# Optimization experiments

Hardware: AMD Instinct MI355X
Metric: run time of the kernel (lower is better)

## Reference

```python
import jax, jax.numpy as jnp
import numpy as np

ALPHA = 0.1
K = 10
N_NODES = 100000
N_EDGES = 3200000


def setup_inputs() -> dict:
    key = jax.random.key(0)
    ks = jax.random.split(key, 8)
    feat = jax.random.normal(ks[0], (N_NODES, 512), dtype=jnp.float32)
    W1 = jax.random.normal(ks[1], (512, 256), dtype=jnp.float32) * (1.0 / np.sqrt(512))
    b1 = jnp.zeros((256,), dtype=jnp.float32)
    W2 = jax.random.normal(ks[2], (256, 64), dtype=jnp.float32) * (1.0 / np.sqrt(256))
    b2 = jnp.zeros((64,), dtype=jnp.float32)
    edge_vals = jax.random.uniform(ks[3], (N_EDGES,), dtype=jnp.float32) / 32.0  # ~row-normalized
    edge_row = jax.random.randint(ks[4], (N_EDGES,), 0, N_NODES, dtype=jnp.int32)
    edge_col = jax.random.randint(ks[5], (N_EDGES,), 0, N_NODES, dtype=jnp.int32)
    return {"features": feat, "W1": W1, "b1": b1, "W2": W2, "b2": b2,
            "edge_vals": edge_vals, "edge_row": edge_row, "edge_col": edge_col}


def _spmm(edge_vals, edge_row, edge_col, x):
    # out[r] = sum_e vals[e] * x[col[e]]  for edges with row[e]==r
    msgs = edge_vals[:, None] * x[edge_col]  # [E, C]
    return jax.ops.segment_sum(msgs, edge_row, num_segments=N_NODES)


def reference(features, W1, b1, W2, b2, edge_vals, edge_row, edge_col):
    # MLP (dropout is identity in eval mode)
    x = jax.nn.relu(features @ W1 + b1)        # [N, nhid]
    x = x @ W2 + b2                             # [N, num_classes]
    h = x
    for _ in range(K):
        x = (1.0 - ALPHA) * _spmm(edge_vals, edge_row, edge_col, x) + ALPHA * h
    return jax.nn.log_softmax(x, axis=1)
```

## Files before the change

kernel.cpp:

```cpp
#include <hip/hip_runtime.h>
#include <hip/hip_bf16.h>
#include <math.h>

#define NNODES 100000
#define NFEAT 512
#define NHID 256
#define NCLS 64
#define ALPHA_C 0.1f
#define NBUCKET 512
#define NPB 512
#define RB2 196

typedef short s16x8 __attribute__((ext_vector_type(8)));
typedef float f32x4 __attribute__((ext_vector_type(4)));

__device__ inline unsigned short f2b(float f) {
    union { float f; unsigned u; } v; v.f = f;
    unsigned r = v.u + 0x7fff + ((v.u >> 16) & 1);
    return (unsigned short)(r >> 16);
}
__device__ inline float b2f(unsigned short b) {
    return __uint_as_float((unsigned)b << 16);
}
__device__ inline float blo(unsigned u) { return __uint_as_float(u << 16); }
__device__ inline float bhi(unsigned u) { return __uint_as_float(u & 0xffff0000u); }

__global__ __launch_bounds__(256) void cvtT_kernel(
    const float* __restrict__ src, unsigned short* __restrict__ dst, int R, int Clog2)
{
    int idx = blockIdx.x * 256 + threadIdx.x;
    int C = 1 << Clog2;
    if (idx < R * C) {
        int r = idx >> Clog2, c = idx & (C - 1);
        dst[(size_t)c * R + r] = f2b(src[idx]);
    }
}

#define HID_STRIDE 264

__global__ __launch_bounds__(256) void mlp_mfma_kernel(
    const float* __restrict__ feat, const unsigned short* __restrict__ W1T,
    const float* __restrict__ b1, const unsigned short* __restrict__ W2T,
    const float* __restrict__ b2, unsigned short* __restrict__ h, int N)
{
    __shared__ unsigned short hid_s[64 * HID_STRIDE];
    const int tid  = threadIdx.x;
    const int w    = tid >> 6;
    const int lane = tid & 63;
    const int lr   = lane & 15;
    const int lh   = lane >> 4;
    const int m0   = blockIdx.x * 64;

    f32x4 acc[4][4];
#pragma unroll
    for (int i = 0; i < 4; ++i)
#pragma unroll
        for (int j = 0; j < 4; ++j) acc[i][j] = (f32x4)0.f;

    const float* arow[4];
#pragma unroll
    for (int mi = 0; mi < 4; ++mi) {
        int r = m0 + mi * 16 + lr;
        if (r > N - 1) r = N - 1;
        arow[mi] = feat + (size_t)r * NFEAT;
    }
    const unsigned short* brow[4];
#pragma unroll
    for (int nj = 0; nj < 4; ++nj)
        brow[nj] = W1T + (size_t)(w * 64 + nj * 16 + lr) * NFEAT;

    for (int kb = 0; kb < NFEAT; kb += 32) {
        const int k0 = kb + lh * 8;
        s16x8 afr[4], bfr[4];
#pragma unroll
        for (int mi = 0; mi < 4; ++mi) {
            float4 f0 = *reinterpret_cast<const float4*>(arow[mi] + k0);
            float4 f1 = *reinterpret_cast<const float4*>(arow[mi] + k0 + 4);
            s16x8 a;
            a[0] = f2b(f0.x); a[1] = f2b(f0.y); a[2] = f2b(f0.z); a[3] = f2b(f0.w);
            a[4] = f2b(f1.x); a[5] = f2b(f1.y); a[6] = f2b(f1.z); a[7] = f2b(f1.w);
            afr[mi] = a;
        }
#pragma unroll
        for (int nj = 0; nj < 4; ++nj)
            bfr[nj] = *reinterpret_cast<const s16x8*>(brow[nj] + k0);
#pragma unroll
        for (int mi = 0; mi < 4; ++mi)
#pragma unroll
            for (int nj = 0; nj < 4; ++nj)
                acc[mi][nj] = __builtin_amdgcn_mfma_f32_16x16x32_bf16(
                    afr[mi], bfr[nj], acc[mi][nj], 0, 0, 0);
    }

#pragma unroll
    for (int nj = 0; nj < 4; ++nj) {
        int col = w * 64 + nj * 16 + lr;
        float bias = b1[col];
#pragma unroll
        for (int mi = 0; mi < 4; ++mi)
#pragma unroll
            for (int q = 0; q < 4; ++q) {
                int row = mi * 16 + lh * 4 + q;
                hid_s[row * HID_STRIDE + col] = f2b(fmaxf(acc[mi][nj][q] + bias, 0.f));
            }
    }
    __syncthreads();

    f32x4 acc2[4];
#pragma unroll
    for (int i = 0; i < 4; ++i) acc2[i] = (f32x4)0.f;
    const int cw = w * 16;
    const unsigned short* b2row = W2T + (size_t)(cw + lr) * NHID;
    for (int ks = 0; ks < NHID; ks += 32) {
        int k0 = ks + lh * 8;
        s16x8 bfr = *reinterpret_cast<const s16x8*>(b2row + k0);
#pragma unroll
        for (int mi = 0; mi < 4; ++mi) {
            s16x8 afr = *reinterpret_cast<const s16x8*>(
                &hid_s[(mi * 16 + lr) * HID_STRIDE + k0]);
            acc2[mi] = __builtin_amdgcn_mfma_f32_16x16x32_bf16(afr, bfr, acc2[mi], 0, 0, 0);
        }
    }
    int col = cw + lr;
    float bias2 = b2[col];
#pragma unroll
    for (int mi = 0; mi < 4; ++mi)
#pragma unroll
        for (int q = 0; q < 4; ++q) {
            int row = m0 + mi * 16 + lh * 4 + q;
            if (row < N) h[(size_t)row * NCLS + col] = f2b(acc2[mi][q] + bias2);
        }
}

__global__ __launch_bounds__(1024) void scanA_kernel(
    const int* __restrict__ cnt, int* __restrict__ excl, int* __restrict__ partials, int n)
{
    __shared__ int wsum[16];
    const int t = threadIdx.x, wid = t >> 6, lane = t & 63;
    const int i = blockIdx.x * 1024 + t;
    int c = (i < n) ? cnt[i] : 0;
    int x = c;
#pragma unroll
    for (int off = 1; off < 64; off <<= 1) {
        int y = __shfl_up(x, off);
        if (lane >= off) x += y;
    }
    if (lane == 63) wsum[wid] = x;
    __syncthreads();
    if (wid == 0 && lane < 16) {
        int wv = wsum[lane];
#pragma unroll
        for (int off = 1; off < 16; off <<= 1) {
            int y = __shfl_up(wv, off);
            if (lane >= off) wv += y;
        }
        wsum[lane] = wv;
    }
    __syncthreads();
    int woff = wid ? wsum[wid - 1] : 0;
    int incl = x + woff;
    if (i < n) excl[i] = incl - c;
    if (t == 1023) partials[blockIdx.x] = incl;
}

__global__ __launch_bounds__(256) void scanB_kernel(
    int* __restrict__ partials, int* __restrict__ total_out, int nb, int n)
{
    __shared__ int s[256];
    const int t = threadIdx.x;
    int v = (t < nb) ? partials[t] : 0;
    s[t] = v;
    __syncthreads();
    for (int off = 1; off < 256; off <<= 1) {
        int y = (t >= off) ? s[t - off] : 0;
        __syncthreads();
        s[t] += y;
        __syncthreads();
    }
    partials[t] = s[t] - v;
    if (t == 255) total_out[n] = s[255];
}

__global__ __launch_bounds__(1024) void scanC_kernel(
    int* __restrict__ arr, const int* __restrict__ partials, int n)
{
    const int i = blockIdx.x * 1024 + threadIdx.x;
    if (i < n) arr[i] += partials[blockIdx.x];
}

__global__ __launch_bounds__(256) void countP1_kernel(
    const int* __restrict__ erow, int* __restrict__ cnts, int E, int CE)
{
    __shared__ int c[NBUCKET];
    const int blk = blockIdx.x, t = threadIdx.x;
    for (int i = t; i < NBUCKET; i += 256) c[i] = 0;
    __syncthreads();
    const int e0 = blk * CE, e1 = min(e0 + CE, E);
    for (int e = e0 + t; e < e1; e += 256)
        atomicAdd(&c[erow[e] / RB2], 1);
    __syncthreads();
    for (int b = t; b < NBUCKET; b += 256)
        cnts[(size_t)b * NPB + blk] = c[b];
}

__global__ __launch_bounds__(256) void scatterA_kernel(
    const float* __restrict__ vals, const int* __restrict__ erow,
    const int* __restrict__ ecol, const int* __restrict__ S,
    unsigned long long* __restrict__ stage, int E, int CE)
{
    __shared__ int lcur[NBUCKET];
    const int blk = blockIdx.x, t = threadIdx.x;
    for (int b = t; b < NBUCKET; b += 256) lcur[b] = S[(size_t)b * NPB + blk];
    __syncthreads();
    const int e0 = blk * CE, e1 = min(e0 + CE, E);
    for (int e = e0 + t; e < e1; e += 256) {
        int r = erow[e];
        unsigned q = (unsigned)__float2int_rn(vals[e] * 1048576.f);
        if (q > 32767u) q = 32767u;
        unsigned lo = ((unsigned)ecol[e] << 15) | q;
        int pos = atomicAdd(&lcur[r / RB2], 1);
        stage[pos] = ((unsigned long long)(unsigned)r << 32) | lo;
    }
}

__global__ __launch_bounds__(256) void scatterB_kernel(
    const unsigned long long* __restrict__ stage, const int* __restrict__ S,
    unsigned* __restrict__ ep, int* __restrict__ row_ptr, int n, int E)
{
    __shared__ int hcnt[256];
    __shared__ int lcur[256];
    const int b = blockIdx.x, t = threadIdx.x;
    if (b == 0 && t == 0) row_ptr[n] = E;
    const int r0 = b * RB2;
    if (r0 >= n) return;
    const int nr = min(RB2, n - r0);
    const int s0 = S[(size_t)b * NPB];
    const int s1 = S[(size_t)(b + 1) * NPB];
    hcnt[t] = 0;
    __syncthreads();
    for (int i = s0 + t; i < s1; i += 256)
        atomicAdd(&hcnt[(int)(stage[i] >> 32) - r0], 1);
    __syncthreads();
    int v = hcnt[t];
    lcur[t] = v;
    __syncthreads();
    for (int off = 1; off < 256; off <<= 1) {
        int y = (t >= off) ? lcur[t - off] : 0;
        __syncthreads();
        lcur[t] += y;
        __syncthreads();
    }
    int excl = lcur[t] - v;
    if (t < nr) row_ptr[r0 + t] = s0 + excl;
    __syncthreads();
    lcur[t] = s0 + excl;
    __syncthreads();
    for (int i = s0 + t; i < s1; i += 256) {
        unsigned long long rec = stage[i];
        int p = atomicAdd(&lcur[(int)(rec >> 32) - r0], 1);
        ep[p] = (unsigned)rec;
    }
}

__global__ __launch_bounds__(256) void spmm_kernel(
    const unsigned short* __restrict__ x_in, const unsigned short* __restrict__ h,
    unsigned short* __restrict__ x_out, const int* __restrict__ row_ptr,
    const unsigned* __restrict__ ep, int n)
{
    const int wid = threadIdx.x >> 6, lane = threadIdx.x & 63;
    const int r = blockIdx.x * 4 + wid;
    if (r >= n) return;
    const int g  = lane >> 4;
    const int li = lane & 15;
    const int s = row_ptr[r], e_end = row_ptr[r + 1];

    float aA0 = 0.f, aA1 = 0.f, aA2 = 0.f, aA3 = 0.f;
    float aB0 = 0.f, aB1 = 0.f, aB2 = 0.f, aB3 = 0.f;
    float aC0 = 0.f, aC1 = 0.f, aC2 = 0.f, aC3 = 0.f;
    float aD0 = 0.f, aD1 = 0.f, aD2 = 0.f, aD3 = 0.f;
    int e0 = s;
    for (; e0 + 16 <= e_end; e0 += 16) {
        unsigned p1 = __builtin_nontemporal_load(ep + e0 + g);
        unsigned p2 = __builtin_nontemporal_load(ep + e0 + 4 + g);
        unsigned p3 = __builtin_nontemporal_load(ep + e0 + 8 + g);
        unsigned p4 = __builtin_nontemporal_load(ep + e0 + 12 + g);
        int   c1 = (int)(p1 >> 15);
        int   c2 = (int)(p2 >> 15);
        int   c3 = (int)(p3 >> 15);
        int   c4 = (int)(p4 >> 15);
        float v1 = (float)(p1 & 0x7fffu) * (1.f / 1048576.f);
        float v2 = (float)(p2 & 0x7fffu) * (1.f / 1048576.f);
        float v3 = (float)(p3 & 0x7fffu) * (1.f / 1048576.f);
        float v4 = (float)(p4 & 0x7fffu) * (1.f / 1048576.f);
        uint2 u1 = *reinterpret_cast<const uint2*>(x_in + ((size_t)c1 << 6) + (li << 2));
        uint2 u2 = *reinterpret_cast<const uint2*>(x_in + ((size_t)c2 << 6) + (li << 2));
        uint2 u3 = *reinterpret_cast<const uint2*>(x_in + ((size_t)c3 << 6) + (li << 2));
        uint2 u4 = *reinterpret_cast<const uint2*>(x_in + ((size_t)c4 << 6) + (li << 2));
        aA0 += v1 * blo(u1.x); aA1 += v1 * bhi(u1.x);
        aA2 += v1 * blo(u1.y); aA3 += v1 * bhi(u1.y);
        aB0 += v2 * blo(u2.x); aB1 += v2 * bhi(u2.x);
        aB2 += v2 * blo(u2.y); aB3 += v2 * bhi(u2.y);
        aC0 += v3 * blo(u3.x); aC1 += v3 * bhi(u3.x);
        aC2 += v3 * blo(u3.y); aC3 += v3 * bhi(u3.y);
        aD0 += v4 * blo(u4.x); aD1 += v4 * bhi(u4.x);
        aD2 += v4 * blo(u4.y); aD3 += v4 * bhi(u4.y);
    }
    for (; e0 < e_end; e0 += 4) {
        int e = e0 + g;
        if (e < e_end) {
            unsigned p = __builtin_nontemporal_load(ep + e);
            int   c = (int)(p >> 15);
            float v = (float)(p & 0x7fffu) * (1.f / 1048576.f);
            uint2 u = *reinterpret_cast<const uint2*>(x_in + ((size_t)c << 6) + (li << 2));
            aA0 += v * blo(u.x); aA1 += v * bhi(u.x);
            aA2 += v * blo(u.y); aA3 += v * bhi(u.y);
        }
    }
    float a0 = (aA0 + aB0) + (aC0 + aD0);
    float a1 = (aA1 + aB1) + (aC1 + aD1);
    float a2 = (aA2 + aB2) + (aC2 + aD2);
    float a3 = (aA3 + aB3) + (aC3 + aD3);
#pragma unroll
    for (int off = 16; off < 64; off <<= 1) {
        a0 += __shfl_xor(a0, off);
        a1 += __shfl_xor(a1, off);
        a2 += __shfl_xor(a2, off);
        a3 += __shfl_xor(a3, off);
    }
    if (g == 0) {
        size_t o = ((size_t)r << 6) + (li << 2);
        const unsigned* hp = reinterpret_cast<const unsigned*>(h + o);
        unsigned hx = __builtin_nontemporal_load(hp);
        unsigned hy = __builtin_nontemporal_load(hp + 1);
        float r0 = (1.f - ALPHA_C) * a0 + ALPHA_C * blo(hx);
        float r1 = (1.f - ALPHA_C) * a1 + ALPHA_C * bhi(hx);
        float r2 = (1.f - ALPHA_C) * a2 + ALPHA_C * blo(hy);
        float r3 = (1.f - ALPHA_C) * a3 + ALPHA_C * bhi(hy);
        uint2 ou;
        ou.x = ((unsigned)f2b(r1) << 16) | f2b(r0);
        ou.y = ((unsigned)f2b(r3) << 16) | f2b(r2);
        *reinterpret_cast<uint2*>(x_out + o) = ou;
    }
}

__global__ __launch_bounds__(256) void lsm_kernel(
    const unsigned short* __restrict__ x, float* __restrict__ out, int n)
{
    const int wid = threadIdx.x >> 6, lane = threadIdx.x & 63;
    const int r = blockIdx.x * 4 + wid;
    if (r >= n) return;
    float v = b2f(x[(size_t)r * NCLS + lane]);
    float m = v;
#pragma unroll
    for (int o = 32; o > 0; o >>= 1) m = fmaxf(m, __shfl_xor(m, o));
    float ex = expf(v - m);
    float s = ex;
#pragma unroll
    for (int o = 32; o > 0; o >>= 1) s += __shfl_xor(s, o);
    out[(size_t)r * NCLS + lane] = (v - m) - logf(s);
}

extern "C" void kernel_launch(void* const* d_in, const int* in_sizes, int n_in,
                              void* d_out, int out_size, void* d_ws, size_t ws_size,
                              hipStream_t stream)
{
    const float* feat = (const float*)d_in[0];
    const float* W1   = (const float*)d_in[1];
    const float* b1   = (const float*)d_in[2];
    const float* W2   = (const float*)d_in[3];
    const float* b2   = (const float*)d_in[4];
    const float* vals = (const float*)d_in[5];
    const int*   erow = (const int*)d_in[6];
    const int*   ecol = (const int*)d_in[7];
    const int N = in_sizes[0] / NFEAT;
    const int E = in_sizes[5];
    float* out = (float*)d_out;
    const int CE = (E + NPB - 1) / NPB;
    const int NC = NBUCKET * NPB;

    size_t off = 0;
    auto alloc = [&](size_t bytes) -> void* {
        void* p = (char*)d_ws + off;
        off += (bytes + 255) & ~(size_t)255;
        return p;
    };
    unsigned short*     h        = (unsigned short*)alloc((size_t)N * NCLS * 2);
    unsigned short*     xA       = (unsigned short*)alloc((size_t)N * NCLS * 2);
    unsigned short*     xB       = (unsigned short*)alloc((size_t)N * NCLS * 2);
    int*                row_ptr  = (int*)alloc((size_t)(N + 1) * 4);
    int*                cnts     = (int*)alloc((size_t)NC * 4);
    int*                S        = (int*)alloc((size_t)(NC + 1) * 4);
    int*                partials = (int*)alloc(256 * 4);
    unsigned*           ep       = (unsigned*)alloc((size_t)E * 4);
    unsigned long long* stage    = (unsigned long long*)alloc((size_t)E * 8);
    unsigned short*     W1T      = (unsigned short*)alloc((size_t)NHID * NFEAT * 2);
    unsigned short*     W2T      = (unsigned short*)alloc((size_t)NCLS * NHID * 2);
    (void)ws_size;

    cvtT_kernel<<<(NFEAT * NHID + 255) / 256, 256, 0, stream>>>(W1, W1T, NFEAT, 8);
    cvtT_kernel<<<(NHID * NCLS + 255) / 256, 256, 0, stream>>>(W2, W2T, NHID, 6);

    mlp_mfma_kernel<<<(N + 63) / 64, 256, 0, stream>>>(feat, W1T, b1, W2T, b2, h, N);

    countP1_kernel<<<NPB, 256, 0, stream>>>(erow, cnts, E, CE);
    scanA_kernel<<<NC / 1024, 1024, 0, stream>>>(cnts, S, partials, NC);
    scanB_kernel<<<1, 256, 0, stream>>>(partials, S, 256, NC);
    scanC_kernel<<<NC / 1024, 1024, 0, stream>>>(S, partials, NC);
    scatterA_kernel<<<NPB, 256, 0, stream>>>(vals, erow, ecol, S, stage, E, CE);
    scatterB_kernel<<<NBUCKET, 256, 0, stream>>>(stage, S, ep, row_ptr, N, E);

    const int gprop = (N + 3) / 4;
    const unsigned short* cur = h;
    for (int i = 0; i < 10; ++i) {
        unsigned short* dst = (i & 1) ? xB : xA;
        spmm_kernel<<<gprop, 256, 0, stream>>>(cur, h, dst, row_ptr, ep, N);
        cur = dst;
    }

    lsm_kernel<<<(N + 3) / 4, 256, 0, stream>>>(cur, out, N);
}
```

Baseline: 1.076 ms.

## Fuse log-softmax into final SpMM, unroll edge loop, use packed bf16 convert

Result: no change. 1.067 ms (-0.8%).

```diff
diff --git a/kernel.cpp b/kernel.cpp
--- a/kernel.cpp
+++ b/kernel.cpp
@@ -24,6 +24,11 @@
 }
 __device__ inline float blo(unsigned u) { return __uint_as_float(u << 16); }
 __device__ inline float bhi(unsigned u) { return __uint_as_float(u & 0xffff0000u); }
+__device__ inline unsigned cvtpk(float a, float b) {
+    unsigned r;
+    asm("v_cvt_pk_bf16_f32 %0, %1, %2" : "=v"(r) : "v"(a), "v"(b));
+    return r;
+}
 
 __global__ __launch_bounds__(256) void cvtT_kernel(
     const float* __restrict__ src, unsigned short* __restrict__ dst, int R, int Clog2)
@@ -76,10 +81,12 @@
         for (int mi = 0; mi < 4; ++mi) {
             float4 f0 = *reinterpret_cast<const float4*>(arow[mi] + k0);
             float4 f1 = *reinterpret_cast<const float4*>(arow[mi] + k0 + 4);
-            s16x8 a;
-            a[0] = f2b(f0.x); a[1] = f2b(f0.y); a[2] = f2b(f0.z); a[3] = f2b(f0.w);
-            a[4] = f2b(f1.x); a[5] = f2b(f1.y); a[6] = f2b(f1.z); a[7] = f2b(f1.w);
-            afr[mi] = a;
+            union { s16x8 v; unsigned u[4]; } cv;
+            cv.u[0] = cvtpk(f0.x, f0.y);
+            cv.u[1] = cvtpk(f0.z, f0.w);
+            cv.u[2] = cvtpk(f1.x, f1.y);
+            cv.u[3] = cvtpk(f1.z, f1.w);
+            afr[mi] = cv.v;
         }
 #pragma unroll
         for (int nj = 0; nj < 4; ++nj)
@@ -257,15 +264,17 @@
     __syncthreads();
     for (int i = s0 + t; i < s1; i += 256) {
         unsigned long long rec = stage[i];
-        int p = atomicAdd(&lcur[(int)(rec >> 32) - r0], 1);
+        int r = (int)(rec >> 32);
+        int p = atomicAdd(&lcur[r - r0], 1);
         ep[p] = (unsigned)rec;
     }
 }
 
+template<int LAST>
 __global__ __launch_bounds__(256) void spmm_kernel(
     const unsigned short* __restrict__ x_in, const unsigned short* __restrict__ h,
-    unsigned short* __restrict__ x_out, const int* __restrict__ row_ptr,
-    const unsigned* __restrict__ ep, int n)
+    unsigned short* __restrict__ x_out, float* __restrict__ out,
+    const int* __restrict__ row_ptr, const unsigned* __restrict__ ep, int n)
 {
     const int wid = threadIdx.x >> 6, lane = threadIdx.x & 63;
     const int r = blockIdx.x * 4 + wid;
@@ -279,23 +288,61 @@
     float aC0 = 0.f, aC1 = 0.f, aC2 = 0.f, aC3 = 0.f;
     float aD0 = 0.f, aD1 = 0.f, aD2 = 0.f, aD3 = 0.f;
     int e0 = s;
+    for (; e0 + 32 <= e_end; e0 += 32) {
+        unsigned p1 = __builtin_nontemporal_load(ep + e0 + g);
+        unsigned p2 = __builtin_nontemporal_load(ep + e0 + 4 + g);
+        unsigned p3 = __builtin_nontemporal_load(ep + e0 + 8 + g);
+        unsigned p4 = __builtin_nontemporal_load(ep + e0 + 12 + g);
+        unsigned p5 = __builtin_nontemporal_load(ep + e0 + 16 + g);
+        unsigned p6 = __builtin_nontemporal_load(ep + e0 + 20 + g);
+        unsigned p7 = __builtin_nontemporal_load(ep + e0 + 24 + g);
+        unsigned p8 = __builtin_nontemporal_load(ep + e0 + 28 + g);
+        uint2 u1 = *reinterpret_cast<const uint2*>(x_in + ((size_t)(p1 >> 15) << 6) + (li << 2));
+        uint2 u2 = *reinterpret_cast<const uint2*>(x_in + ((size_t)(p2 >> 15) << 6) + (li << 2));
+        uint2 u3 = *reinterpret_cast<const uint2*>(x_in + ((size_t)(p3 >> 15) << 6) + (li << 2));
+        uint2 u4 = *reinterpret_cast<const uint2*>(x_in + ((size_t)(p4 >> 15) << 6) + (li << 2));
+        uint2 u5 = *reinterpret_cast<const uint2*>(x_in + ((size_t)(p5 >> 15) << 6) + (li << 2));
+        uint2 u6 = *reinterpret_cast<const uint2*>(x_in + ((size_t)(p6 >> 15) << 6) + (li << 2));
+        uint2 u7 = *reinterpret_cast<const uint2*>(x_in + ((size_t)(p7 >> 15) << 6) + (li << 2));
+        uint2 u8 = *reinterpret_cast<const uint2*>(x_in + ((size_t)(p8 >> 15) << 6) + (li << 2));
+        float v1 = (float)(p1 & 0x7fffu) * (1.f / 1048576.f);
+        float v2 = (float)(p2 & 0x7fffu) * (1.f / 1048576.f);
+        float v3 = (float)(p3 & 0x7fffu) * (1.f / 1048576.f);
+        float v4 = (float)(p4 & 0x7fffu) * (1.f / 1048576.f);
+        float v5 = (float)(p5 & 0x7fffu) * (1.f / 1048576.f);
+        float v6 = (float)(p6 & 0x7fffu) * (1.f / 1048576.f);
+        float v7 = (float)(p7 & 0x7fffu) * (1.f / 1048576.f);
+        float v8 = (float)(p8 & 0x7fffu) * (1.f / 1048576.f);
+        aA0 += v1 * blo(u1.x); aA1 += v1 * bhi(u1.x);
+        aA2 += v1 * blo(u1.y); aA3 += v1 * bhi(u1.y);
+        aB0 += v2 * blo(u2.x); aB1 += v2 * bhi(u2.x);
+        aB2 += v2 * blo(u2.y); aB3 += v2 * bhi(u2.y);
+        aC0 += v3 * blo(u3.x); aC1 += v3 * bhi(u3.x);
+        aC2 += v3 * blo(u3.y); aC3 += v3 * bhi(u3.y);
+        aD0 += v4 * blo(u4.x); aD1 += v4 * bhi(u4.x);
+        aD2 += v4 * blo(u4.y); aD3 += v4 * bhi(u4.y);
+        aA0 += v5 * blo(u5.x); aA1 += v5 * bhi(u5.x);
+        aA2 += v5 * blo(u5.y); aA3 += v5 * bhi(u5.y);
+        aB0 += v6 * blo(u6.x); aB1 += v6 * bhi(u6.x);
+        aB2 += v6 * blo(u6.y); aB3 += v6 * bhi(u6.y);
+        aC0 += v7 * blo(u7.x); aC1 += v7 * bhi(u7.x);
+        aC2 += v7 * blo(u7.y); aC3 += v7 * bhi(u7.y);
+        aD0 += v8 * blo(u8.x); aD1 += v8 * bhi(u8.x);
+        aD2 += v8 * blo(u8.y); aD3 += v8 * bhi(u8.y);
+    }
     for (; e0 + 16 <= e_end; e0 += 16) {
         unsigned p1 = __builtin_nontemporal_load(ep + e0 + g);
         unsigned p2 = __builtin_nontemporal_load(ep + e0 + 4 + g);
         unsigned p3 = __builtin_nontemporal_load(ep + e0 + 8 + g);
         unsigned p4 = __builtin_nontemporal_load(ep + e0 + 12 + g);
-        int   c1 = (int)(p1 >> 15);
-        int   c2 = (int)(p2 >> 15);
-        int   c3 = (int)(p3 >> 15);
-        int   c4 = (int)(p4 >> 15);
+        uint2 u1 = *reinterpret_cast<const uint2*>(x_in + ((size_t)(p1 >> 15) << 6) + (li << 2));
+        uint2 u2 = *reinterpret_cast<const uint2*>(x_in + ((size_t)(p2 >> 15) << 6) + (li << 2));
+        uint2 u3 = *reinterpret_cast<const uint2*>(x_in + ((size_t)(p3 >> 15) << 6) + (li << 2));
+        uint2 u4 = *reinterpret_cast<const uint2*>(x_in + ((size_t)(p4 >> 15) << 6) + (li << 2));
         float v1 = (float)(p1 & 0x7fffu) * (1.f / 1048576.f);
         float v2 = (float)(p2 & 0x7fffu) * (1.f / 1048576.f);
         float v3 = (float)(p3 & 0x7fffu) * (1.f / 1048576.f);
         float v4 = (float)(p4 & 0x7fffu) * (1.f / 1048576.f);
-        uint2 u1 = *reinterpret_cast<const uint2*>(x_in + ((size_t)c1 << 6) + (li << 2));
-        uint2 u2 = *reinterpret_cast<const uint2*>(x_in + ((size_t)c2 << 6) + (li << 2));
-        uint2 u3 = *reinterpret_cast<const uint2*>(x_in + ((size_t)c3 << 6) + (li << 2));
-        uint2 u4 = *reinterpret_cast<const uint2*>(x_in + ((size_t)c4 << 6) + (li << 2));
         aA0 += v1 * blo(u1.x); aA1 += v1 * bhi(u1.x);
         aA2 += v1 * blo(u1.y); aA3 += v1 * bhi(u1.y);
         aB0 += v2 * blo(u2.x); aB1 += v2 * bhi(u2.x);
@@ -336,28 +383,26 @@
         float r1 = (1.f - ALPHA_C) * a1 + ALPHA_C * bhi(hx);
         float r2 = (1.f - ALPHA_C) * a2 + ALPHA_C * blo(hy);
         float r3 = (1.f - ALPHA_C) * a3 + ALPHA_C * bhi(hy);
-        uint2 ou;
-        ou.x = ((unsigned)f2b(r1) << 16) | f2b(r0);
-        ou.y = ((unsigned)f2b(r3) << 16) | f2b(r2);
-        *reinterpret_cast<uint2*>(x_out + o) = ou;
-    }
-}
-
-__global__ __launch_bounds__(256) void lsm_kernel(
-    const unsigned short* __restrict__ x, float* __restrict__ out, int n)
-{
-    const int wid = threadIdx.x >> 6, lane = threadIdx.x & 63;
-    const int r = blockIdx.x * 4 + wid;
-    if (r >= n) return;
-    float v = b2f(x[(size_t)r * NCLS + lane]);
-    float m = v;
-#pragma unroll
-    for (int o = 32; o > 0; o >>= 1) m = fmaxf(m, __shfl_xor(m, o));
-    float ex = expf(v - m);
-    float s = ex;
-#pragma unroll
-    for (int o = 32; o > 0; o >>= 1) s += __shfl_xor(s, o);
-    out[(size_t)r * NCLS + lane] = (v - m) - logf(s);
+        if (LAST) {
+            float m = fmaxf(fmaxf(r0, r1), fmaxf(r2, r3));
+#pragma unroll
+            for (int off = 1; off < 16; off <<= 1) m = fmaxf(m, __shfl_xor(m, off));
+            float sum = expf(r0 - m) + expf(r1 - m) + expf(r2 - m) + expf(r3 - m);
+#pragma unroll
+            for (int off = 1; off < 16; off <<= 1) sum += __shfl_xor(sum, off);
+            float ls = logf(sum);
+            float4 ov;
+            ov.x = (r0 - m) - ls;
+            ov.y = (r1 - m) - ls;
+            ov.z = (r2 - m) - ls;
+            ov.w = (r3 - m) - ls;
+            *reinterpret_cast<float4*>(out + o) = ov;
+        } else {
+            unsigned* op = reinterpret_cast<unsigned*>(x_out + o);
+            __builtin_nontemporal_store(((unsigned)f2b(r1) << 16) | f2b(r0), op);
+            __builtin_nontemporal_store(((unsigned)f2b(r3) << 16) | f2b(r2), op + 1);
+        }
+    }
 }
 
 extern "C" void kernel_launch(void* const* d_in, const int* in_sizes, int n_in,
@@ -411,11 +456,10 @@
 
     const int gprop = (N + 3) / 4;
     const unsigned short* cur = h;
-    for (int i = 0; i < 10; ++i) {
+    for (int i = 0; i < 9; ++i) {
         unsigned short* dst = (i & 1) ? xB : xA;
-        spmm_kernel<<<gprop, 256, 0, stream>>>(cur, h, dst, row_ptr, ep, N);
+        spmm_kernel<0><<<gprop, 256, 0, stream>>>(cur, h, dst, nullptr, row_ptr, ep, N);
         cur = dst;
     }
-
-    lsm_kernel<<<(N + 3) / 4, 256, 0, stream>>>(cur, out, N);
-}
+    spmm_kernel<1><<<gprop, 256, 0, stream>>>(cur, h, nullptr, out, row_ptr, ep, N);
+}
```
